# Optimization experiments

Hardware: AMD Instinct MI355X
Metric: run time of the kernel (lower is better)

## Reference

```python
import jax, jax.numpy as jnp
import numpy as np

SCALE = 2
PAD = 4
EPS = 1e-5
K = 5
N, C, H, W = 4, 64, 128, 128


def _splits(a, s):
    # (..., W, H) -> (..., W/s, H/s, s*s), block decimation matching torch view/permute
    *lead, Wd, Hd = a.shape
    b = a.reshape(*lead, s, Wd // s, s, Hd // s)
    nl = len(lead)
    b = jnp.transpose(b, tuple(range(nl)) + (nl + 1, nl + 3, nl, nl + 2))
    return b.reshape(*lead, Wd // s, Hd // s, s * s)


def _p2o(psf, Hs, Ws):
    # PSF -> OTF: zero-pad, roll to center at origin, FFT
    kh, kw = psf.shape[-2], psf.shape[-1]
    otf = jnp.zeros(psf.shape[:-2] + (Hs, Ws), psf.dtype).at[..., :kh, :kw].set(psf)
    otf = jnp.roll(otf, (-(kh // 2), -(kw // 2)), axis=(-2, -1))
    return jnp.fft.fftn(otf, axes=(-2, -1))


def _upsample(x, s):
    # s-fold zero-filling upsampler (S^T y)
    n, c, h, w = x.shape
    return jnp.zeros((n, c, h * s, w * s), x.dtype).at[..., ::s, ::s].set(x)


def setup_inputs() -> dict:
    key = jax.random.key(0)
    kx, kw_, _ = jax.random.split(key, 3)
    x = jax.random.normal(kx, (N, C, H, W), dtype=jnp.float32)
    w_raw = jax.random.normal(kw_, (1, C, K, K), dtype=jnp.float32)
    weight = jax.nn.softmax(w_raw.reshape(1, C, -1), axis=-1).reshape(1, C, K, K)
    bias = jnp.zeros((1, C, 1, 1), dtype=jnp.float32)
    return {"x": x, "weight": weight, "bias": bias}


def reference(x, weight, bias):
    s = SCALE
    xp = jnp.pad(x, ((0, 0), (0, 0), (PAD, PAD), (PAD, PAD)), mode="wrap")  # circular
    biaseps = jax.nn.sigmoid(bias - 9.0) + EPS  # (1,C,1,1)
    _, _, h, w = xp.shape
    STy = _upsample(xp, s)  # zero-filled upsample
    # nearest-neighbor interpolate by integer factor s
    xn = jnp.repeat(jnp.repeat(xp, s, axis=-2), s, axis=-1)
    FB = _p2o(weight, h * s, w * s)           # (1,C,hs,ws) complex
    FBC = jnp.conj(FB)
    F2B = jnp.abs(FB) ** 2                     # real
    FBFy = FBC * jnp.fft.fftn(STy, axes=(-2, -1))
    FR = FBFy + jnp.fft.fftn(biaseps * xn, axes=(-2, -1))
    x1 = FB * FR
    FBR = jnp.mean(_splits(x1, s), axis=-1)    # (N,C,h,w) complex
    invW = jnp.mean(_splits(F2B, s), axis=-1)  # (1,C,h,w) real
    invWBR = FBR / (invW + biaseps)
    FCBinvWBR = FBC * jnp.tile(invWBR, (1, 1, s, s))
    FX = (FR - FCBinvWBR) / biaseps
    out = jnp.real(jnp.fft.ifftn(FX, axes=(-2, -1)))
    out = out[..., PAD * s:-PAD * s, PAD * s:-PAD * s]
    return out
```

## Files before the change

kernel.cpp:

```cpp
#include <hip/hip_runtime.h>
#include <math.h>


#define MDIM 136
#define RSC  70
#define HC   69
#define PLANE_HALF (MDIM*HC)
#define NPLANES 256
#define LDS_CPLX2 (2*MDIM*RSC + 2*MDIM)
#define PI_D 3.14159265358979323846
#define NTH 1024

__device__ __forceinline__ int slot136(int k) { return 17*(k & 7) + (k >> 3); }
__device__ __forceinline__ int slot68(int k)  { return 17*(k & 3) + (k >> 2); }

template<int DIR, class F>
__device__ __forceinline__ void dft17_sink(float2* z, int base, int stride, F f)
{
    constexpr float C17[9] = {1.f, 0.93247223f, 0.73900892f, 0.44573836f,
                              0.09226836f, -0.27366299f, -0.60263464f,
                              -0.85021714f, -0.98297310f};
    constexpr float S17[9] = {0.f, 0.36124167f, 0.67369564f, 0.89516329f,
                              0.99573418f, 0.96182564f, 0.79801723f,
                              0.52643216f, 0.18374952f};
    constexpr float d = (DIR > 0) ? 1.f : -1.f;
    float xr[17], xi[17];
#pragma unroll
    for (int n = 0; n < 17; n++) {
        float2 v = z[base + n*stride];
        xr[n] = v.x; xi[n] = v.y;
    }
    float ar[8], ai[8], br[8], bi[8];
#pragma unroll
    for (int n = 1; n <= 8; n++) {
        ar[n-1] = xr[n] + xr[17-n];  ai[n-1] = xi[n] + xi[17-n];
        br[n-1] = xr[n] - xr[17-n];  bi[n-1] = xi[n] - xi[17-n];
    }
    float s0r = xr[0], s0i = xi[0];
#pragma unroll
    for (int n = 0; n < 8; n++) { s0r += ar[n]; s0i += ai[n]; }
    f(0, s0r, s0i);
#pragma unroll
    for (int k = 1; k <= 8; k++) {
        float Pr = xr[0], Pi = xi[0], Qr = 0.f, Qi = 0.f;
#pragma unroll
        for (int n = 1; n <= 8; n++) {
            int m = (k*n) % 17;
            float cc = (m <= 8) ? C17[m] : C17[17-m];
            float ss = (m <= 8) ? S17[m] : -S17[17-m];
            Pr = fmaf(ar[n-1], cc, Pr);
            Pi = fmaf(ai[n-1], cc, Pi);
            Qr = fmaf(br[n-1], ss, Qr);
            Qi = fmaf(bi[n-1], ss, Qi);
        }
        f(k,    Pr - d*Qi, Pi + d*Qr);
        f(17-k, Pr + d*Qi, Pi - d*Qr);
    }
}

template<int DIR>
__device__ __forceinline__ void radix4_tw(float2* z, const float2* lut, int base, int n2,
                                          float2 Z0, float2 Z1, float2 Z2, float2 Z3)
{
    constexpr float d = (DIR > 0) ? 1.0f : -1.0f;
    float t0r = Z0.x+Z2.x, t0i = Z0.y+Z2.y;
    float t1r = Z0.x-Z2.x, t1i = Z0.y-Z2.y;
    float t2r = Z1.x+Z3.x, t2i = Z1.y+Z3.y;
    float t3r = Z1.x-Z3.x, t3i = Z1.y-Z3.y;
    float X0r = t0r+t2r,     X0i = t0i+t2i;
    float X2r = t0r-t2r,     X2i = t0i-t2i;
    float X1r = t1r - d*t3i, X1i = t1i + d*t3r;
    float X3r = t1r + d*t3i, X3i = t1i - d*t3r;
    z[base + n2] = make_float2(X0r, X0i);
    float2 w1 = lut[2*n2], w2 = lut[4*n2], w3 = lut[6*n2];
    z[base + 17 + n2] = make_float2(X1r*w1.x - X1i*w1.y, X1r*w1.y + X1i*w1.x);
    z[base + 34 + n2] = make_float2(X2r*w2.x - X2i*w2.y, X2r*w2.y + X2i*w2.x);
    z[base + 51 + n2] = make_float2(X3r*w3.x - X3i*w3.y, X3r*w3.y + X3i*w3.x);
}

template<int DIR>
__device__ __forceinline__ void fft136_s1_body(float2* z, const float2* lut,
                                               int c, int n2)
{
    constexpr float d = (DIR > 0) ? 1.0f : -1.0f;
    constexpr float C707 = 0.70710678118654752f;
    float xr[8], xi[8];
#pragma unroll
    for (int n1 = 0; n1 < 8; n1++) {
        float2 v = z[(17*n1 + n2)*RSC + c];
        xr[n1] = v.x; xi[n1] = v.y;
    }
    float e0r = xr[0]+xr[4], e0i = xi[0]+xi[4];
    float e1r = xr[0]-xr[4], e1i = xi[0]-xi[4];
    float o0r = xr[2]+xr[6], o0i = xi[2]+xi[6];
    float o1r = xr[2]-xr[6], o1i = xi[2]-xi[6];
    float E0r = e0r+o0r, E0i = e0i+o0i;
    float E2r = e0r-o0r, E2i = e0i-o0i;
    float E1r = e1r - d*o1i, E1i = e1i + d*o1r;
    float E3r = e1r + d*o1i, E3i = e1i - d*o1r;
    float f0r = xr[1]+xr[5], f0i = xi[1]+xi[5];
    float f1r = xr[1]-xr[5], f1i = xi[1]-xi[5];
    float h0r = xr[3]+xr[7], h0i = xi[3]+xi[7];
    float h1r = xr[3]-xr[7], h1i = xi[3]-xi[7];
    float O0r = f0r+h0r, O0i = f0i+h0i;
    float O2r = f0r-h0r, O2i = f0i-h0i;
    float O1r = f1r - d*h1i, O1i = f1i + d*h1r;
    float O3r = f1r + d*h1i, O3i = f1i - d*h1r;
    float t1r =  C707*(O1r - d*O1i), t1i = C707*(O1i + d*O1r);
    float t2r = -d*O2i,              t2i = d*O2r;
    float t3r = -C707*(O3r + d*O3i), t3i = C707*(d*O3r - O3i);
    float Xr[8], Xi[8];
    Xr[0]=E0r+O0r; Xi[0]=E0i+O0i;  Xr[4]=E0r-O0r; Xi[4]=E0i-O0i;
    Xr[1]=E1r+t1r; Xi[1]=E1i+t1i;  Xr[5]=E1r-t1r; Xi[5]=E1i-t1i;
    Xr[2]=E2r+t2r; Xi[2]=E2i+t2i;  Xr[6]=E2r-t2r; Xi[6]=E2i-t2i;
    Xr[3]=E3r+t3r; Xi[3]=E3i+t3i;  Xr[7]=E3r-t3r; Xi[7]=E3i-t3i;
    z[n2*RSC + c] = make_float2(Xr[0], Xi[0]);
    int ti = 0;
#pragma unroll
    for (int k1 = 1; k1 < 8; k1++) {
        ti += n2;
        float2 w = lut[ti];
        z[(17*k1 + n2)*RSC + c] = make_float2(Xr[k1]*w.x - Xi[k1]*w.y,
                                              Xr[k1]*w.y + Xi[k1]*w.x);
    }
}

template<int DIR>
__device__ void fft136_s1(float2* z, const float2* lut, int ncols, int tid)
{
    int c = tid / 17;
    int n2 = tid - c*17;
    for (int e = tid; e < ncols*17; e += NTH) {
        fft136_s1_body<DIR>(z, lut, c, n2);
        c += 60; n2 += 4; if (n2 >= 17) { n2 -= 17; c++; }
    }
}

template<int DIR>
__device__ void ct68_s1(float2* z, const float2* lut, int tid)
{
    int row = tid / 17;
    int n2  = tid - row*17;
    for (int e = tid; e < MDIM*17; e += NTH) {
        int base = row*RSC;
        float2 Z0 = z[base + n2];
        float2 Z1 = z[base + 17 + n2];
        float2 Z2 = z[base + 34 + n2];
        float2 Z3 = z[base + 51 + n2];
        radix4_tw<DIR>(z, lut, base, n2, Z0, Z1, Z2, Z3);
        row += 60; n2 += 4; if (n2 >= 17) { n2 -= 17; row++; }
    }
}

__device__ __forceinline__ float2 c2r_pack(float2 a, float2 b, float2 w)
{
    float Sr = a.x + b.x, Si = a.y - b.y;
    float Dr = a.x - b.x, Di = a.y + b.y;
    float Or = w.x*Dr - w.y*Di, Oi = w.x*Di + w.y*Dr;
    return make_float2(Sr - Oi, Si + Or);
}

__global__ __launch_bounds__(1024, 4) void conv_kernel(const float* __restrict__ x,
                                                       const float2* __restrict__ Abuf,
                                                       float* __restrict__ out)
{
    extern __shared__ float2 zsm[];
    float2* z0   = zsm;
    float2* z1   = zsm + MDIM*RSC;
    float2* lutI = zsm + 2*MDIM*RSC;
    float2* lutF = lutI + MDIM;
    const int tid = threadIdx.x;
    const int nc  = blockIdx.x;
    const int c   = nc & 63;

    if (tid < MDIM) {
        float s, cc; sincosf(2.0f*(float)PI_D*(float)tid/136.0f, &s, &cc);
        lutI[tid] = make_float2(cc, s);
        lutF[tid] = make_float2(cc, -s);
    }
    const float* xp = x + (size_t)nc * (128*128);
    {
        int i = tid / 68, n = tid - (tid/68)*68;
        for (int e = tid; e < MDIM*68; e += NTH) {
            int si = (i + 124) & 127;
            int j0 = (2*n + 124) & 127;
            z0[i*RSC + n] = *reinterpret_cast<const float2*>(xp + si*128 + j0);
            i += 15; n += 4; if (n >= 68) { n -= 68; i++; }
        }
    }
    __syncthreads();
    ct68_s1<-1>(z0, lutF, tid);
    __syncthreads();
    if (tid < MDIM*4) {
        int row = tid >> 2, k1 = tid & 3;
        int base = row*RSC + 17*k1;
        dft17_sink<-1>(z0, base, 1, [&](int k2, float re, float im) {
            z0[base + k2] = make_float2(re, im);
        });
    }
    __syncthreads();
    {
        int row = tid / 35, k = tid - (tid/35)*35;
        for (int e = tid; e < MDIM*35; e += NTH) {
            int base = row*RSC;
            int sa = slot68(k);
            float2 Za = z0[base+sa];
            float Zar = Za.x, Zai = Za.y;
            float Zbr, Zbi; int sb;
            if (k == 0) { Zbr = Zar; Zbi = Zai; sb = 68; }
            else {
                int kk = 68-k; sb = slot68(kk);
                float2 Zb = z0[base+sb]; Zbr = Zb.x; Zbi = Zb.y;
            }
            float2 w = lutF[k];
            float wc = w.x, ws = w.y;
            float Er = 0.5f*(Zar + Zbr), Ei = 0.5f*(Zai - Zbi);
            float Dr = 0.5f*(Zar - Zbr), Di = 0.5f*(Zai + Zbi);
            float Tr = wc*Dr - ws*Di, Ti = wc*Di + ws*Dr;
            z0[base+sa] = make_float2(Er + Ti, Ei - Tr);
            float E2r = Er,  E2i = -Ei;
            float D2r = -Dr, D2i = Di;
            float w2c = -wc, w2s = ws;
            float T2r = w2c*D2r - w2s*D2i, T2i = w2c*D2i + w2s*D2r;
            z0[base+sb] = make_float2(E2r + T2i, E2i - T2r);
            row += 29; k += 9; if (k >= 35) { k -= 35; row++; }
        }
    }
    __syncthreads();
    fft136_s1<-1>(z0, lutF, HC, tid);
    __syncthreads();
    if (tid < HC*8) {
        int cc = tid >> 3, k1 = tid & 7;
        int base = 17*k1*RSC + cc;
        dft17_sink<-1>(z0, base, RSC, [&](int k2, float re, float im) {
            z0[base + k2*RSC] = make_float2(re, im);
        });
    }
    __syncthreads();
    float2 Xreg[10];
    {
        int g1 = tid / HC, g2 = tid - (tid/HC)*HC;
#pragma unroll
        for (int k = 0; k < 10; k++) {
            if (k < 9 || tid < PLANE_HALF - 9*NTH) {
                int cq = (g2 == 68) ? 68 : slot68(g2);
                Xreg[k] = z0[slot136(g1)*RSC + cq];
            }
            g1 += 14; g2 += 58; if (g2 >= HC) { g2 -= HC; g1++; }
        }
    }
    __syncthreads();
    float* op = out + (size_t)nc * (256*256);
#pragma unroll 1
    for (int u = 0; u < 2; u++) {
        const float2* A0 = Abuf + (size_t)(c*4 + u*2) * PLANE_HALF;
        const float2* A1 = A0 + PLANE_HALF;
        {
            int g1 = tid / HC, g2 = tid - (tid/HC)*HC;
#pragma unroll
            for (int k = 0; k < 10; k++) {
                if (k < 9 || tid < PLANE_HALF - 9*NTH) {
                    int e = tid + k*NTH;
                    float2 xv = Xreg[k];
                    float2 a0 = A0[e], a1 = A1[e];
                    int a = g1*RSC + g2;
                    z0[a] = make_float2(a0.x*xv.x - a0.y*xv.y, a0.x*xv.y + a0.y*xv.x);
                    z1[a] = make_float2(a1.x*xv.x - a1.y*xv.y, a1.x*xv.y + a1.y*xv.x);
                }
                g1 += 14; g2 += 58; if (g2 >= HC) { g2 -= HC; g1++; }
            }
        }
        __syncthreads();
        for (int it = tid; it < 2*HC*17; it += NTH) {
            int pl = it >= HC*17;
            int ee = it - (pl ? HC*17 : 0);
            int cc = (ee*241) >> 12;
            int n2 = ee - cc*17;
            fft136_s1_body<1>(pl ? z1 : z0, lutI, cc, n2);
        }
        __syncthreads();
        for (int it = tid; it < 2*HC*8; it += NTH) {
            int pl = it >= HC*8;
            int i  = it - (pl ? HC*8 : 0);
            float2* zz = pl ? z1 : z0;
            int cc = i >> 3, k1 = i & 7;
            int base = 17*k1*RSC + cc;
            dft17_sink<1>(zz, base, RSC, [&](int k2, float re, float im) {
                zz[base + k2*RSC] = make_float2(re, im);
            });
        }
        __syncthreads();
        for (int it = tid; it < 2*MDIM*9; it += NTH) {
            int pl = it >= MDIM*9;
            int i  = it - (pl ? MDIM*9 : 0);
            float2* zz = pl ? z1 : z0;
            int row = (i*7282) >> 16;
            int g   = i - row*9;
            int base = row*RSC;
            if (g == 0) {
                float2 T0  = zz[base],    T17 = zz[base+17], T34 = zz[base+34],
                       T51 = zz[base+51], T68 = zz[base+68];
                float2 Z0 = c2r_pack(T0,  T68, lutI[0]);
                float2 Z1 = c2r_pack(T17, T51, lutI[17]);
                float2 Z2 = c2r_pack(T34, T34, lutI[34]);
                float2 Z3 = c2r_pack(T51, T17, lutI[51]);
                radix4_tw<1>(zz, lutI, base, 0, Z0, Z1, Z2, Z3);
            } else {
                int gb = 17 - g;
                float2 Ta0 = zz[base+g],    Ta1 = zz[base+g+17],
                       Ta2 = zz[base+g+34], Ta3 = zz[base+g+51];
                float2 Tb0 = zz[base+gb],    Tb1 = zz[base+gb+17],
                       Tb2 = zz[base+gb+34], Tb3 = zz[base+gb+51];
                float2 Za0 = c2r_pack(Ta0, Tb3, lutI[g]);
                float2 Za1 = c2r_pack(Ta1, Tb2, lutI[g+17]);
                float2 Za2 = c2r_pack(Ta2, Tb1, lutI[g+34]);
                float2 Za3 = c2r_pack(Ta3, Tb0, lutI[g+51]);
                float2 Zb0 = c2r_pack(Tb0, Ta3, lutI[gb]);
                float2 Zb1 = c2r_pack(Tb1, Ta2, lutI[gb+17]);
                float2 Zb2 = c2r_pack(Tb2, Ta1, lutI[gb+34]);
                float2 Zb3 = c2r_pack(Tb3, Ta0, lutI[gb+51]);
                radix4_tw<1>(zz, lutI, base, g,  Za0, Za1, Za2, Za3);
                radix4_tw<1>(zz, lutI, base, gb, Zb0, Zb1, Zb2, Zb3);
            }
        }
        __syncthreads();
        for (int it = tid; it < 2*MDIM*4; it += NTH) {
            int pl = it >= MDIM*4;
            int i  = it - (pl ? MDIM*4 : 0);
            float2* zz = pl ? z1 : z0;
            int row = i >> 2, k1 = i & 3;
            int base = row*RSC + 17*k1;
            dft17_sink<1>(zz, base, 1, [&](int k2, float re, float im) {
                zz[base + k2] = make_float2(re, im);
            });
        }
        __syncthreads();
        {
            int m  = 2 + (tid & 63);
            int y1 = 4 + (tid >> 6);
            int a  = slot136(y1)*RSC + slot68(m);
            float* rowp = op + (size_t)(2*y1 + u - 8)*256 + 4*m - 8;
#pragma unroll
            for (int it = 0; it < 8; ++it) {
                float2 w0 = z0[a], w1 = z1[a];
                *reinterpret_cast<float4*>(rowp) = make_float4(w0.x, w1.x, w0.y, w1.y);
                a += 2*RSC;
                rowp += 32*256;
            }
        }
        __syncthreads();
    }
}

__global__ void prep_kernel(const float* __restrict__ weight,
                            const float* __restrict__ bias,
                            float2* __restrict__ Abuf)
{
    __shared__ double tabc[272], tabs[272];
    __shared__ double Rs[69*5*4];
    for (int t = threadIdx.x; t < 272; t += blockDim.x) {
        double s, c; sincos(-2.0*PI_D*(double)t/272.0, &s, &c);
        tabc[t] = c; tabs[t] = s;
    }
    const int c     = blockIdx.x >> 3;
    const int chunk = blockIdx.x & 7;
    const float* wp = weight + c*25;
    const double r = 1.0/(1.0 + exp(9.0 - (double)bias[c])) + 1e-5;
    __syncthreads();
    for (int it = threadIdx.x; it < 69*5; it += blockDim.x) {
        int g2 = it / 5, a = it - 5*g2;
        double c2 = tabc[g2], s2 = tabs[g2];
        double e2r[5], e2i[5];
        e2r[2]=1.0; e2i[2]=0.0; e2r[3]=c2; e2i[3]=s2;
        e2r[4]=c2*c2-s2*s2; e2i[4]=2.0*c2*s2;
        e2r[1]=c2; e2i[1]=-s2; e2r[0]=e2r[4]; e2i[0]=-e2i[4];
        double w0=wp[a*5+0], w1=wp[a*5+1], w2=wp[a*5+2], w3=wp[a*5+3], w4=wp[a*5+4];
        double Rer = w0*e2r[0] + w2*e2r[2] + w4*e2r[4];
        double Rei = w0*e2i[0] + w2*e2i[2] + w4*e2i[4];
        double Ror = w1*e2r[1] + w3*e2r[3];
        double Roi = w1*e2i[1] + w3*e2i[3];
        Rs[it*4+0] = Rer + Ror;  Rs[it*4+1] = Rei + Roi;
        Rs[it*4+2] = Rer - Ror;  Rs[it*4+3] = Rei - Roi;
    }
    __syncthreads();

    const int e_lo = chunk * 1173;
    const int e_hi = e_lo + 1173;
    int e  = e_lo + (int)threadIdx.x;
    int g1 = e / HC, g2 = e - (e/HC)*HC;
    for (; e < e_hi; e += blockDim.x) {
        double c1 = tabc[g1], s1 = tabs[g1];
        double e1r[5], e1i[5];
        e1r[2]=1.0; e1i[2]=0.0; e1r[3]=c1; e1i[3]=s1;
        e1r[4]=c1*c1-s1*s1; e1i[4]=2.0*c1*s1;
        e1r[1]=c1; e1i[1]=-s1; e1r[0]=e1r[4]; e1i[0]=-e1i[4];

        double FBr[2][2], FBi[2][2];
#pragma unroll
        for (int b1 = 0; b1 < 2; b1++) {
            double Per=0, Pei=0, Por=0, Poi=0;
#pragma unroll
            for (int a = 0; a < 5; a++) {
                double Rr = Rs[(g2*5+a)*4 + 2*b1];
                double Ri = Rs[(g2*5+a)*4 + 2*b1 + 1];
                double tr = e1r[a]*Rr - e1i[a]*Ri;
                double ti = e1r[a]*Ri + e1i[a]*Rr;
                if (a & 1) { Por += tr; Poi += ti; } else { Per += tr; Pei += ti; }
            }
            FBr[0][b1] = Per + Por;  FBi[0][b1] = Pei + Poi;
            FBr[1][b1] = Per - Por;  FBi[1][b1] = Pei - Poi;
        }
        double c2 = tabc[g2], s2 = tabs[g2];
        double ur[2]={1.0+c1, 1.0-c1}, ui[2]={s1, -s1};
        double vr[2]={1.0+c2, 1.0-c2}, vi[2]={s2, -s2};
        double Br_[2][2], Bi_[2][2];
#pragma unroll
        for (int a1 = 0; a1 < 2; a1++)
#pragma unroll
            for (int b1 = 0; b1 < 2; b1++) {
                Br_[a1][b1] = ur[a1]*vr[b1] - ui[a1]*vi[b1];
                Bi_[a1][b1] = ur[a1]*vi[b1] + ui[a1]*vr[b1];
            }
        double invW=0, Qr=0, Qi=0;
#pragma unroll
        for (int a1 = 0; a1 < 2; a1++)
#pragma unroll
            for (int b1 = 0; b1 < 2; b1++) {
                invW += FBr[a1][b1]*FBr[a1][b1] + FBi[a1][b1]*FBi[a1][b1];
                Qr += FBr[a1][b1]*Br_[a1][b1] - FBi[a1][b1]*Bi_[a1][b1];
                Qi += FBr[a1][b1]*Bi_[a1][b1] + FBi[a1][b1]*Br_[a1][b1];
            }
        invW *= 0.25; Qr *= 0.25; Qi *= 0.25;
        double den = 1.0/(invW + r);
        double Sr = (1.0 - Qr)*den, Si = -Qi*den;
        double Mr[2][2], Mi[2][2];
#pragma unroll
        for (int a1 = 0; a1 < 2; a1++)
#pragma unroll
            for (int b1 = 0; b1 < 2; b1++) {
                Mr[a1][b1] = Br_[a1][b1] + FBr[a1][b1]*Sr + FBi[a1][b1]*Si;
                Mi[a1][b1] = Bi_[a1][b1] + FBr[a1][b1]*Si - FBi[a1][b1]*Sr;
            }
        const double scale = 1.0/73984.0;
#pragma unroll
        for (int uu = 0; uu < 2; uu++)
#pragma unroll
            for (int vv = 0; vv < 2; vv++) {
                double sr=0, si=0;
#pragma unroll
                for (int a1 = 0; a1 < 2; a1++)
#pragma unroll
                    for (int b1 = 0; b1 < 2; b1++) {
                        if ((a1*uu + b1*vv) & 1) { sr -= Mr[a1][b1]; si -= Mi[a1][b1]; }
                        else                     { sr += Mr[a1][b1]; si += Mi[a1][b1]; }
                    }
                int t = g1*uu + g2*vv;
                double pc = tabc[t], ps = -tabs[t];
                float2 outv;
                outv.x = (float)((pc*sr - ps*si)*scale);
                outv.y = (float)((pc*si + ps*sr)*scale);
                Abuf[((size_t)(c*4 + uu*2 + vv))*PLANE_HALF + e] = outv;
            }
        g1 += 3; g2 += 49; if (g2 >= HC) { g2 -= HC; g1++; }
    }
}

extern "C" void kernel_launch(void* const* d_in, const int* in_sizes, int n_in,
                              void* d_out, int out_size, void* d_ws, size_t ws_size,
                              hipStream_t stream)
{
    const float* x      = (const float*)d_in[0];
    const float* weight = (const float*)d_in[1];
    const float* bias   = (const float*)d_in[2];
    float* out = (float*)d_out;

    float2* Abuf = (float2*)d_ws;

    const size_t lds_conv = (size_t)LDS_CPLX2 * sizeof(float2);
    (void)hipFuncSetAttribute((const void*)conv_kernel,
                              hipFuncAttributeMaxDynamicSharedMemorySize, (int)lds_conv);

    prep_kernel<<<512, 256, 0, stream>>>(weight, bias, Abuf);
    conv_kernel<<<NPLANES, 1024, lds_conv, stream>>>(x, Abuf, out);
}
```

Baseline: 140.7 us.

## Prefetch spectral multiplier planes into registers and use contiguous per-stage twiddle tables

Loads of the per-channel multiplier planes from global memory move ahead of the forward FFT stage and the next iteration's inverse FFT stage, held in registers, so their latency overlaps LDS FFT work. The kernel also adds small LDS twiddle tables laid out per radix stage, indexed contiguously by (k1,n2), replacing strided lookups into the single 136-entry table and avoiding bank conflicts. The cost is 40 extra float2 registers per thread, which risks spills or lower occupancy with 1024-thread blocks.

Measured after the change: 153.8 us. +9.3%, slower.

```diff
diff --git a/kernel.cpp b/kernel.cpp
--- a/kernel.cpp
+++ b/kernel.cpp
@@ -7,7 +7,7 @@
 #define HC   69
 #define PLANE_HALF (MDIM*HC)
 #define NPLANES 256
-#define LDS_CPLX2 (2*MDIM*RSC + 2*MDIM)
+#define LDS_CPLX2 (2*MDIM*RSC + 2*MDIM + 2*119 + 2*51)
 #define PI_D 3.14159265358979323846
 #define NTH 1024
 
@@ -59,7 +59,7 @@
 }
 
 template<int DIR>
-__device__ __forceinline__ void radix4_tw(float2* z, const float2* lut, int base, int n2,
+__device__ __forceinline__ void radix4_tw(float2* z, const float2* t68, int base, int n2,
                                           float2 Z0, float2 Z1, float2 Z2, float2 Z3)
 {
     constexpr float d = (DIR > 0) ? 1.0f : -1.0f;
@@ -72,14 +72,14 @@
     float X1r = t1r - d*t3i, X1i = t1i + d*t3r;
     float X3r = t1r + d*t3i, X3i = t1i - d*t3r;
     z[base + n2] = make_float2(X0r, X0i);
-    float2 w1 = lut[2*n2], w2 = lut[4*n2], w3 = lut[6*n2];
+    float2 w1 = t68[n2], w2 = t68[17 + n2], w3 = t68[34 + n2];
     z[base + 17 + n2] = make_float2(X1r*w1.x - X1i*w1.y, X1r*w1.y + X1i*w1.x);
     z[base + 34 + n2] = make_float2(X2r*w2.x - X2i*w2.y, X2r*w2.y + X2i*w2.x);
     z[base + 51 + n2] = make_float2(X3r*w3.x - X3i*w3.y, X3r*w3.y + X3i*w3.x);
 }
 
 template<int DIR>
-__device__ __forceinline__ void fft136_s1_body(float2* z, const float2* lut,
+__device__ __forceinline__ void fft136_s1_body(float2* z, const float2* t136,
                                                int c, int n2)
 {
     constexpr float d = (DIR > 0) ? 1.0f : -1.0f;
@@ -115,29 +115,27 @@
     Xr[2]=E2r+t2r; Xi[2]=E2i+t2i;  Xr[6]=E2r-t2r; Xi[6]=E2i-t2i;
     Xr[3]=E3r+t3r; Xi[3]=E3i+t3i;  Xr[7]=E3r-t3r; Xi[7]=E3i-t3i;
     z[n2*RSC + c] = make_float2(Xr[0], Xi[0]);
-    int ti = 0;
 #pragma unroll
     for (int k1 = 1; k1 < 8; k1++) {
-        ti += n2;
-        float2 w = lut[ti];
+        float2 w = t136[(k1-1)*17 + n2];
         z[(17*k1 + n2)*RSC + c] = make_float2(Xr[k1]*w.x - Xi[k1]*w.y,
                                               Xr[k1]*w.y + Xi[k1]*w.x);
     }
 }
 
 template<int DIR>
-__device__ void fft136_s1(float2* z, const float2* lut, int ncols, int tid)
+__device__ void fft136_s1(float2* z, const float2* t136, int ncols, int tid)
 {
     int c = tid / 17;
     int n2 = tid - c*17;
     for (int e = tid; e < ncols*17; e += NTH) {
-        fft136_s1_body<DIR>(z, lut, c, n2);
+        fft136_s1_body<DIR>(z, t136, c, n2);
         c += 60; n2 += 4; if (n2 >= 17) { n2 -= 17; c++; }
     }
 }
 
 template<int DIR>
-__device__ void ct68_s1(float2* z, const float2* lut, int tid)
+__device__ void ct68_s1(float2* z, const float2* t68, int tid)
 {
     int row = tid / 17;
     int n2  = tid - row*17;
@@ -147,7 +145,7 @@
         float2 Z1 = z[base + 17 + n2];
         float2 Z2 = z[base + 34 + n2];
         float2 Z3 = z[base + 51 + n2];
-        radix4_tw<DIR>(z, lut, base, n2, Z0, Z1, Z2, Z3);
+        radix4_tw<DIR>(z, t68, base, n2, Z0, Z1, Z2, Z3);
         row += 60; n2 += 4; if (n2 >= 17) { n2 -= 17; row++; }
     }
 }
@@ -165,10 +163,14 @@
                                                        float* __restrict__ out)
 {
     extern __shared__ float2 zsm[];
-    float2* z0   = zsm;
-    float2* z1   = zsm + MDIM*RSC;
-    float2* lutI = zsm + 2*MDIM*RSC;
-    float2* lutF = lutI + MDIM;
+    float2* z0    = zsm;
+    float2* z1    = zsm + MDIM*RSC;
+    float2* lutI  = zsm + 2*MDIM*RSC;
+    float2* lutF  = lutI + MDIM;
+    float2* tI136 = lutF + MDIM;
+    float2* tF136 = tI136 + 119;
+    float2* tI68  = tF136 + 119;
+    float2* tF68  = tI68 + 51;
     const int tid = threadIdx.x;
     const int nc  = blockIdx.x;
     const int c   = nc & 63;
@@ -177,6 +179,18 @@
         float s, cc; sincosf(2.0f*(float)PI_D*(float)tid/136.0f, &s, &cc);
         lutI[tid] = make_float2(cc, s);
         lutF[tid] = make_float2(cc, -s);
+    } else if (tid < MDIM + 119) {
+        int it = tid - MDIM;
+        int k1 = it/17 + 1, n2 = it - (it/17)*17;
+        float s, cc; sincosf((float)(PI_D/68.0)*(float)(k1*n2), &s, &cc);
+        tI136[it] = make_float2(cc, s);
+        tF136[it] = make_float2(cc, -s);
+    } else if (tid < MDIM + 119 + 51) {
+        int it = tid - MDIM - 119;
+        int j = it/17, n2 = it - 17*j;
+        float s, cc; sincosf((float)(PI_D/34.0)*(float)((j+1)*n2), &s, &cc);
+        tI68[it] = make_float2(cc, s);
+        tF68[it] = make_float2(cc, -s);
     }
     const float* xp = x + (size_t)nc * (128*128);
     {
@@ -189,7 +203,7 @@
         }
     }
     __syncthreads();
-    ct68_s1<-1>(z0, lutF, tid);
+    ct68_s1<-1>(z0, tF68, tid);
     __syncthreads();
     if (tid < MDIM*4) {
         int row = tid >> 2, k1 = tid & 3;
@@ -227,7 +241,18 @@
         }
     }
     __syncthreads();
-    fft136_s1<-1>(z0, lutF, HC, tid);
+    float2 Ar0[10], Ar1[10];
+    {
+        const float2* A0 = Abuf + (size_t)(c*4) * PLANE_HALF;
+        const float2* A1 = A0 + PLANE_HALF;
+        int e = tid;
+#pragma unroll
+        for (int k = 0; k < 10; k++) {
+            if (k < 9 || tid < PLANE_HALF - 9*NTH) { Ar0[k] = A0[e]; Ar1[k] = A1[e]; }
+            e += NTH;
+        }
+    }
+    fft136_s1<-1>(z0, tF136, HC, tid);
     __syncthreads();
     if (tid < HC*8) {
         int cc = tid >> 3, k1 = tid & 7;
@@ -253,16 +278,13 @@
     float* op = out + (size_t)nc * (256*256);
 #pragma unroll 1
     for (int u = 0; u < 2; u++) {
-        const float2* A0 = Abuf + (size_t)(c*4 + u*2) * PLANE_HALF;
-        const float2* A1 = A0 + PLANE_HALF;
         {
             int g1 = tid / HC, g2 = tid - (tid/HC)*HC;
 #pragma unroll
             for (int k = 0; k < 10; k++) {
                 if (k < 9 || tid < PLANE_HALF - 9*NTH) {
-                    int e = tid + k*NTH;
                     float2 xv = Xreg[k];
-                    float2 a0 = A0[e], a1 = A1[e];
+                    float2 a0 = Ar0[k], a1 = Ar1[k];
                     int a = g1*RSC + g2;
                     z0[a] = make_float2(a0.x*xv.x - a0.y*xv.y, a0.x*xv.y + a0.y*xv.x);
                     z1[a] = make_float2(a1.x*xv.x - a1.y*xv.y, a1.x*xv.y + a1.y*xv.x);
@@ -271,12 +293,22 @@
             }
         }
         __syncthreads();
+        if (u == 0) {
+            const float2* A0 = Abuf + (size_t)(c*4 + 2) * PLANE_HALF;
+            const float2* A1 = A0 + PLANE_HALF;
+            int e = tid;
+#pragma unroll
+            for (int k = 0; k < 10; k++) {
+                if (k < 9 || tid < PLANE_HALF - 9*NTH) { Ar0[k] = A0[e]; Ar1[k] = A1[e]; }
+                e += NTH;
+            }
+        }
         for (int it = tid; it < 2*HC*17; it += NTH) {
             int pl = it >= HC*17;
             int ee = it - (pl ? HC*17 : 0);
             int cc = (ee*241) >> 12;
             int n2 = ee - cc*17;
-            fft136_s1_body<1>(pl ? z1 : z0, lutI, cc, n2);
+            fft136_s1_body<1>(pl ? z1 : z0, tI136, cc, n2);
         }
         __syncthreads();
         for (int it = tid; it < 2*HC*8; it += NTH) {
@@ -304,7 +336,7 @@
                 float2 Z1 = c2r_pack(T17, T51, lutI[17]);
                 float2 Z2 = c2r_pack(T34, T34, lutI[34]);
                 float2 Z3 = c2r_pack(T51, T17, lutI[51]);
-                radix4_tw<1>(zz, lutI, base, 0, Z0, Z1, Z2, Z3);
+                radix4_tw<1>(zz, tI68, base, 0, Z0, Z1, Z2, Z3);
             } else {
                 int gb = 17 - g;
                 float2 Ta0 = zz[base+g],    Ta1 = zz[base+g+17],
@@ -319,8 +351,8 @@
                 float2 Zb1 = c2r_pack(Tb1, Ta2, lutI[gb+17]);
                 float2 Zb2 = c2r_pack(Tb2, Ta1, lutI[gb+34]);
                 float2 Zb3 = c2r_pack(Tb3, Ta0, lutI[gb+51]);
-                radix4_tw<1>(zz, lutI, base, g,  Za0, Za1, Za2, Za3);
-                radix4_tw<1>(zz, lutI, base, gb, Zb0, Zb1, Zb2, Zb3);
+                radix4_tw<1>(zz, tI68, base, g,  Za0, Za1, Za2, Za3);
+                radix4_tw<1>(zz, tI68, base, gb, Zb0, Zb1, Zb2, Zb3);
             }
         }
         __syncthreads();
```
